# Performance work log

Hardware: AMD Instinct MI355X
Metric: run time of the kernel (lower is better)

Reference implementation:

```python
import jax, jax.numpy as jnp
import numpy as np

N = 50000
E = 800000
F_IN = 128
H = 8        # heads
C = 32       # hidden_channels per head
HC = H * C   # 256
NEG_SLOPE = 0.2


def setup_inputs() -> dict:
    key = jax.random.key(0)
    ks = jax.random.split(key, 16)
    s = 0.1
    return {
        'x': jax.random.normal(ks[0], (N, F_IN), jnp.float32),
        'edge_index': jax.random.randint(ks[1], (2, E), 0, N, jnp.int64),
        'edge_weights': jax.random.uniform(ks[2], (E,), jnp.float32),
        'W1': jax.random.normal(ks[3], (F_IN, HC), jnp.float32) * s,
        'att_src1': jax.random.normal(ks[4], (H, C), jnp.float32) * s,
        'att_dst1': jax.random.normal(ks[5], (H, C), jnp.float32) * s,
        'b1': jnp.zeros((HC,), jnp.float32),
        'W2': jax.random.normal(ks[6], (HC, HC), jnp.float32) * s,
        'att_src2': jax.random.normal(ks[7], (H, C), jnp.float32) * s,
        'att_dst2': jax.random.normal(ks[8], (H, C), jnp.float32) * s,
        'b2': jnp.zeros((HC,), jnp.float32),
        'We': jax.random.normal(ks[9], (HC, 1), jnp.float32) * s,
        'be': jnp.zeros((1,), jnp.float32),
        'Wn': jax.random.normal(ks[10], (HC, 1), jnp.float32) * s,
        'bn': jnp.zeros((1,), jnp.float32),
    }


def gat_conv(x, src, dst, W, att_src, att_dst, bias):
    """PyG GATConv (concat=True, eval mode, self-loops already in src/dst)."""
    n = x.shape[0]
    h = (x @ W).reshape(n, H, C)                      # [N,H,C]
    a_s = jnp.sum(h * att_src, axis=-1)               # [N,H]
    a_d = jnp.sum(h * att_dst, axis=-1)               # [N,H]
    e = jax.nn.leaky_relu(a_s[src] + a_d[dst], NEG_SLOPE)  # [E',H]
    m = jax.ops.segment_max(e, dst, num_segments=n)   # segment softmax over dst
    ex = jnp.exp(e - m[dst])
    denom = jax.ops.segment_sum(ex, dst, num_segments=n)
    alpha = ex / (denom[dst] + 1e-16)                 # [E',H]
    out = jax.ops.segment_sum(alpha[..., None] * h[src], dst, num_segments=n)
    return out.reshape(n, HC) + bias


def reference(x, edge_index, edge_weights, W1, att_src1, att_dst1, b1,
              W2, att_src2, att_dst2, b2, We, be, Wn, bn):
    src0, dst0 = edge_index[0], edge_index[1]
    loops = jnp.arange(N, dtype=src0.dtype)
    src = jnp.concatenate([src0, loops])
    dst = jnp.concatenate([dst0, loops])
    # edge_weights is passed to GATConv as edge_attr but unused (edge_dim=None)
    h = jax.nn.relu(gat_conv(x, src, dst, W1, att_src1, att_dst1, b1))
    h = jax.nn.relu(gat_conv(h, src, dst, W2, att_src2, att_dst2, b2))
    edge_pred = (h[src0] * h[dst0]) @ We + be          # [E,1]
    node_pred = h @ Wn + bn                            # [N,1]
    return (edge_pred, node_pred)
```

## Files before the change

### kernel.cpp

```cpp
#include <hip/hip_runtime.h>
#include <hip/hip_bf16.h>

#define NN 50000
#define NE 800000
#define FIN 128
#define HC 256
#define NEG_SLOPE 0.2f

#define GEMM_BLOCKS 1564
#define NSCAT 3328
#define NB_HIST 782
#define NB_X 6250
#define NB_W1 128
#define NB_W2 256

typedef short bf16x8 __attribute__((ext_vector_type(8)));
typedef float f32x4 __attribute__((ext_vector_type(4)));

__device__ __forceinline__ unsigned short f2bf(float f) {
  unsigned u = __float_as_uint(f);
  u += 0x7fff + ((u >> 16) & 1);
  return (unsigned short)(u >> 16);
}
__device__ __forceinline__ float bf2f(unsigned short s) {
  return __uint_as_float((unsigned)s << 16);
}
__device__ __forceinline__ float bflo(unsigned u) { return __uint_as_float(u << 16); }
__device__ __forceinline__ float bfhi(unsigned u) { return __uint_as_float(u & 0xffff0000u); }

__global__ __launch_bounds__(256) void prep_hist(
    const float* __restrict__ X, unsigned short* __restrict__ Xh,
    const float* __restrict__ W1, unsigned short* __restrict__ W1th,
    unsigned short* __restrict__ W1tl, const float* __restrict__ W2,
    unsigned short* __restrict__ W2th, unsigned short* __restrict__ W2tl,
    const int* __restrict__ ei, int* __restrict__ counts) {
  int b = blockIdx.x, t = threadIdx.x;
  if (b < NB_HIST) {
#pragma unroll
    for (int u = 0; u < 4; ++u) {
      int e = b * 1024 + u * 256 + t;
      if (e < NE) atomicAdd(&counts[ei[NE + e]], 1);
    }
  } else if (b < NB_HIST + NB_X) {
    int i = (b - NB_HIST) * 256 + t;
    float4 v = ((const float4*)X)[i];
    ushort4 h;
    h.x = f2bf(v.x); h.y = f2bf(v.y); h.z = f2bf(v.z); h.w = f2bf(v.w);
    ((ushort4*)Xh)[i] = h;
  } else if (b < NB_HIST + NB_X + NB_W1) {
    int j = (b - NB_HIST - NB_X) * 256 + t;
    int n = j >> 7, k = j & 127;
    float v = W1[k * HC + n];
    unsigned short h = f2bf(v);
    W1th[j] = h;
    W1tl[j] = f2bf(v - bf2f(h));
  } else {
    int j = (b - NB_HIST - NB_X - NB_W1) * 256 + t;
    int n = j >> 8, k = j & 255;
    float v = W2[k * HC + n];
    unsigned short h = f2bf(v);
    W2th[j] = h;
    W2tl[j] = f2bf(v - bf2f(h));
  }
}

__global__ __launch_bounds__(256) void gemm_coef(
    const unsigned short* __restrict__ A, const unsigned short* __restrict__ Bth,
    const unsigned short* __restrict__ Btl, const float* __restrict__ att_s,
    const float* __restrict__ att_d, unsigned short* __restrict__ Cb,
    float* __restrict__ a_s, float* __restrict__ a_d, int M, int K,
    const int* __restrict__ ei, const int* __restrict__ rowptr,
    int* __restrict__ tmpc, int2* __restrict__ ce, int scat) {
  __shared__ unsigned short sA[64 * 40];
  __shared__ unsigned short sBh[128 * 40];
  __shared__ unsigned short sBl[128 * 40];
  __shared__ float sCS[64][4];
  __shared__ float sCD[64][4];

  int bid = blockIdx.x, t = threadIdx.x;
  if (bid < scat) {
    int x = bid & 7;
    int c = bid >> 3;
#pragma unroll
    for (int u = 0; u < 8; ++u) {
      int e = c * 2048 + u * 256 + t;
      if (e < NE + NN) {
        int d = (e < NE) ? ei[NE + e] : e - NE;
        if ((unsigned)d / 6250u == (unsigned)x) {
          int s  = (e < NE) ? ei[e] : d;
          int id = (e < NE) ? e : -1;
          int pos = rowptr[d] + atomicAdd(&tmpc[d], 1);
          ce[pos] = make_int2(s, id);
        }
      }
    }
    return;
  }

  int gb = bid - scat;
  int w = t >> 6, lane = t & 63;
  int quad = lane >> 4, lrow = lane & 15;
  int m0 = (gb >> 1) * 64, n0 = (gb & 1) * 128;
  int rm = (w & 1) * 32, cn = (w >> 1) * 64;

  f32x4 acc[2][4] = {};

  for (int k0 = 0; k0 < K; k0 += 32) {
    {
      int row = t >> 2, q = t & 3;
      int gm = m0 + row;
      if (gm >= M) gm = M - 1;
      *(uint4*)(sA + row * 40 + q * 8) = *(const uint4*)(A + (size_t)gm * K + k0 + q * 8);
    }
#pragma unroll
    for (int i = 0; i < 2; ++i) {
      int idx = t + i * 256;
      int row = idx >> 2, q = idx & 3;
      size_t gbx = (size_t)(n0 + row) * K + k0 + q * 8;
      *(uint4*)(sBh + row * 40 + q * 8) = *(const uint4*)(Bth + gbx);
      *(uint4*)(sBl + row * 40 + q * 8) = *(const uint4*)(Btl + gbx);
    }
    __syncthreads();

    bf16x8 fa[2];
#pragma unroll
    for (int mi = 0; mi < 2; ++mi)
      fa[mi] = *(const bf16x8*)(sA + (rm + mi * 16 + lrow) * 40 + quad * 8);
#pragma unroll
    for (int ni = 0; ni < 4; ++ni) {
      bf16x8 fbh = *(const bf16x8*)(sBh + (cn + ni * 16 + lrow) * 40 + quad * 8);
      bf16x8 fbl = *(const bf16x8*)(sBl + (cn + ni * 16 + lrow) * 40 + quad * 8);
#pragma unroll
      for (int mi = 0; mi < 2; ++mi) {
        acc[mi][ni] = __builtin_amdgcn_mfma_f32_16x16x32_bf16(fa[mi], fbh, acc[mi][ni], 0, 0, 0);
        acc[mi][ni] = __builtin_amdgcn_mfma_f32_16x16x32_bf16(fa[mi], fbl, acc[mi][ni], 0, 0, 0);
      }
    }
    __syncthreads();
  }

  float vs[4], vd[4];
#pragma unroll
  for (int ni = 0; ni < 4; ++ni) {
    int gn = n0 + cn + ni * 16 + lrow;
    vs[ni] = att_s[gn];
    vd[ni] = att_d[gn];
  }
  int h4e = cn >> 5;

#pragma unroll
  for (int mi = 0; mi < 2; ++mi) {
#pragma unroll
    for (int r = 0; r < 4; ++r) {
      int lr = rm + mi * 16 + quad * 4 + r;
      int gm = m0 + lr;
      if (gm < M) {
#pragma unroll
        for (int ni = 0; ni < 4; ++ni) {
          int gn = n0 + cn + ni * 16 + lrow;
          Cb[(size_t)gm * HC + gn] = f2bf(acc[mi][ni][r]);
        }
      }
      float pse = acc[mi][0][r] * vs[0] + acc[mi][1][r] * vs[1];
      float pso = acc[mi][2][r] * vs[2] + acc[mi][3][r] * vs[3];
      float pde = acc[mi][0][r] * vd[0] + acc[mi][1][r] * vd[1];
      float pdo = acc[mi][2][r] * vd[2] + acc[mi][3][r] * vd[3];
#pragma unroll
      for (int off = 1; off <= 8; off <<= 1) {
        pse += __shfl_xor(pse, off);
        pso += __shfl_xor(pso, off);
        pde += __shfl_xor(pde, off);
        pdo += __shfl_xor(pdo, off);
      }
      if (lrow == 0) {
        sCS[lr][h4e] = pse;
        sCS[lr][h4e + 1] = pso;
        sCD[lr][h4e] = pde;
        sCD[lr][h4e + 1] = pdo;
      }
    }
  }
  __syncthreads();
  if (t < 64) {
    int gm = m0 + t;
    if (gm < M) {
      int o = (n0 >> 5);
      *(float4*)(a_s + (size_t)gm * 8 + o) = *(const float4*)&sCS[t][0];
      *(float4*)(a_d + (size_t)gm * 8 + o) = *(const float4*)&sCD[t][0];
    }
  }
}

__global__ void scan1(const int* __restrict__ counts, int* __restrict__ scanbuf,
                      int* __restrict__ bsum) {
  __shared__ int sd[256];
  int t = threadIdx.x;
  int i = blockIdx.x * 256 + t;
  int v = (i < NN) ? counts[i] + 1 : 0;
  sd[t] = v;
  __syncthreads();
#pragma unroll
  for (int off = 1; off < 256; off <<= 1) {
    int x = (t >= off) ? sd[t - off] : 0;
    __syncthreads();
    sd[t] += x;
    __syncthreads();
  }
  if (i < NN) scanbuf[i] = sd[t];
  if (t == 255) bsum[blockIdx.x] = sd[255];
}

__global__ void scan2(const int* __restrict__ bsum, int* __restrict__ boff, int nb) {
  __shared__ int sd[256];
  int t = threadIdx.x;
  int v = (t < nb) ? bsum[t] : 0;
  sd[t] = v;
  __syncthreads();
#pragma unroll
  for (int off = 1; off < 256; off <<= 1) {
    int x = (t >= off) ? sd[t - off] : 0;
    __syncthreads();
    sd[t] += x;
    __syncthreads();
  }
  if (t < nb) boff[t] = sd[t] - v;
}

__global__ void scan3(const int* __restrict__ scanbuf, const int* __restrict__ boff,
                      int* __restrict__ rowptr) {
  int i = blockIdx.x * 256 + threadIdx.x;
  if (i < NN) rowptr[i + 1] = scanbuf[i] + boff[blockIdx.x];
  if (i == 0) rowptr[0] = 0;
}

__global__ __launch_bounds__(256) void agg_kernel(
    const unsigned short* __restrict__ htb, const float* __restrict__ a_s,
    const float* __restrict__ a_d, const int* __restrict__ rowptr,
    const int2* __restrict__ ce, const float* __restrict__ bias,
    unsigned short* __restrict__ outb,
    const float* __restrict__ Wn, const float* __restrict__ bn,
    float* __restrict__ outn) {
  int d = blockIdx.x * 4 + (threadIdx.x >> 6);
  if (d >= NN) return;
  int l = threadIdx.x & 63;
  int hh = l >> 3;
  float adh = a_d[d * 8 + hh];
  int r0 = rowptr[d], r1 = rowptr[d + 1];
  float denom = 0.f;
  float4 acc = {0.f, 0.f, 0.f, 0.f};
  for (int r = r0; r < r1; r += 4) {
    int s[4];
    float as_[4];
    uint2 q[4];
    bool ok[4];
#pragma unroll
    for (int j = 0; j < 4; ++j) {
      int rj = r + j;
      ok[j] = rj < r1;
      rj = ok[j] ? rj : r1 - 1;
      s[j] = ce[rj].x;
    }
#pragma unroll
    for (int j = 0; j < 4; ++j) {
      as_[j] = a_s[s[j] * 8 + hh];
      q[j] = ((const uint2*)(htb + (size_t)s[j] * HC))[l];
    }
#pragma unroll
    for (int j = 0; j < 4; ++j) {
      float e = as_[j] + adh;
      e = e > 0.f ? e : NEG_SLOPE * e;
      float w = ok[j] ? __expf(e) : 0.f;
      denom += w;
      acc.x += w * bflo(q[j].x);
      acc.y += w * bfhi(q[j].x);
      acc.z += w * bflo(q[j].y);
      acc.w += w * bfhi(q[j].y);
    }
  }
  float dv = 1.f / denom;
  float4 bi = *(const float4*)(bias + l * 4);
  float4 o;
  o.x = fmaxf(fmaf(acc.x, dv, bi.x), 0.f);
  o.y = fmaxf(fmaf(acc.y, dv, bi.y), 0.f);
  o.z = fmaxf(fmaf(acc.z, dv, bi.z), 0.f);
  o.w = fmaxf(fmaf(acc.w, dv, bi.w), 0.f);
  uint2 pb;
  pb.x = (unsigned)f2bf(o.x) | ((unsigned)f2bf(o.y) << 16);
  pb.y = (unsigned)f2bf(o.z) | ((unsigned)f2bf(o.w) << 16);
  ((uint2*)(outb + (size_t)d * HC))[l] = pb;
  if (outn) {
    float4 wv = *(const float4*)(Wn + l * 4);
    float p = o.x * wv.x + o.y * wv.y + o.z * wv.z + o.w * wv.w;
#pragma unroll
    for (int off = 1; off <= 32; off <<= 1) p += __shfl_xor(p, off);
    if (l == 0) outn[d] = p + bn[0];
  }
}

__global__ __launch_bounds__(256) void edge_pred_kernel(
    const unsigned short* __restrict__ h2b, const int* __restrict__ rowptr,
    const int2* __restrict__ ce, const float* __restrict__ We,
    const float* __restrict__ be, float* __restrict__ out) {
  int d = blockIdx.x * 4 + (threadIdx.x >> 6);
  if (d >= NN) return;
  int lane = threadIdx.x & 63;
  int g = lane >> 4, l = lane & 15;
  float b = be[0];

  const uint4* rowd = (const uint4*)(h2b + (size_t)d * HC + l * 16);
  uint4 qd0 = rowd[0], qd1 = rowd[1];
  float wd[16];
  {
    const float4* wep = (const float4*)(We + l * 16);
    float4 w0 = wep[0], w1 = wep[1], w2 = wep[2], w3 = wep[3];
    wd[0] = bflo(qd0.x) * w0.x;  wd[1] = bfhi(qd0.x) * w0.y;
    wd[2] = bflo(qd0.y) * w0.z;  wd[3] = bfhi(qd0.y) * w0.w;
    wd[4] = bflo(qd0.z) * w1.x;  wd[5] = bfhi(qd0.z) * w1.y;
    wd[6] = bflo(qd0.w) * w1.z;  wd[7] = bfhi(qd0.w) * w1.w;
    wd[8] = bflo(qd1.x) * w2.x;  wd[9] = bfhi(qd1.x) * w2.y;
    wd[10] = bflo(qd1.y) * w2.z; wd[11] = bfhi(qd1.y) * w2.w;
    wd[12] = bflo(qd1.z) * w3.x; wd[13] = bfhi(qd1.z) * w3.y;
    wd[14] = bflo(qd1.w) * w3.z; wd[15] = bfhi(qd1.w) * w3.w;
  }

  int r0 = rowptr[d], r1 = rowptr[d + 1];
  for (int r = r0; r < r1; r += 8) {
    int rr0 = r + g, rr1 = r + 4 + g;
    int s0 = 0, id0 = -1, s1 = 0, id1 = -1;
    if (rr0 < r1) { int2 p = ce[rr0]; s0 = p.x; id0 = p.y; }
    if (rr1 < r1) { int2 p = ce[rr1]; s1 = p.x; id1 = p.y; }
    const uint4* ra = (const uint4*)(h2b + (size_t)s0 * HC + l * 16);
    const uint4* rb = (const uint4*)(h2b + (size_t)s1 * HC + l * 16);
    uint4 a0 = ra[0], a1 = ra[1];
    uint4 c0 = rb[0], c1 = rb[1];
    float p0 = bflo(a0.x) * wd[0] + bfhi(a0.x) * wd[1] + bflo(a0.y) * wd[2] +
               bfhi(a0.y) * wd[3] + bflo(a0.z) * wd[4] + bfhi(a0.z) * wd[5] +
               bflo(a0.w) * wd[6] + bfhi(a0.w) * wd[7] + bflo(a1.x) * wd[8] +
               bfhi(a1.x) * wd[9] + bflo(a1.y) * wd[10] + bfhi(a1.y) * wd[11] +
               bflo(a1.z) * wd[12] + bfhi(a1.z) * wd[13] + bflo(a1.w) * wd[14] +
               bfhi(a1.w) * wd[15];
    float p1 = bflo(c0.x) * wd[0] + bfhi(c0.x) * wd[1] + bflo(c0.y) * wd[2] +
               bfhi(c0.y) * wd[3] + bflo(c0.z) * wd[4] + bfhi(c0.z) * wd[5] +
               bflo(c0.w) * wd[6] + bfhi(c0.w) * wd[7] + bflo(c1.x) * wd[8] +
               bfhi(c1.x) * wd[9] + bflo(c1.y) * wd[10] + bfhi(c1.y) * wd[11] +
               bflo(c1.z) * wd[12] + bfhi(c1.z) * wd[13] + bflo(c1.w) * wd[14] +
               bfhi(c1.w) * wd[15];
#pragma unroll
    for (int off = 1; off <= 8; off <<= 1) {
      p0 += __shfl_xor(p0, off);
      p1 += __shfl_xor(p1, off);
    }
    if (l == 0) {
      if (id0 >= 0) out[id0] = p0 + b;
      if (id1 >= 0) out[id1] = p1 + b;
    }
  }
}

extern "C" void kernel_launch(void* const* d_in, const int* in_sizes, int n_in,
                              void* d_out, int out_size, void* d_ws, size_t ws_size,
                              hipStream_t stream) {
  const float* x  = (const float*)d_in[0];
  const int* ei   = (const int*)d_in[1];
  const float* W1 = (const float*)d_in[3];
  const float* as1 = (const float*)d_in[4];
  const float* ad1 = (const float*)d_in[5];
  const float* b1 = (const float*)d_in[6];
  const float* W2 = (const float*)d_in[7];
  const float* as2 = (const float*)d_in[8];
  const float* ad2 = (const float*)d_in[9];
  const float* b2 = (const float*)d_in[10];
  const float* We = (const float*)d_in[11];
  const float* be = (const float*)d_in[12];
  const float* Wn = (const float*)d_in[13];
  const float* bn = (const float*)d_in[14];
  float* out = (float*)d_out;

  char* wsp = (char*)d_ws;
  auto alloc = [&](size_t bytes) {
    char* p = wsp;
    wsp += (bytes + 255) & ~(size_t)255;
    return p;
  };
  unsigned short* hbA = (unsigned short*)alloc((size_t)NN * HC * 2);
  unsigned short* h1b = (unsigned short*)alloc((size_t)NN * HC * 2);
  unsigned short* hbB = (unsigned short*)alloc((size_t)NN * HC * 2);
  float* a_s = (float*)alloc((size_t)NN * 8 * 4);
  float* a_d = (float*)alloc((size_t)NN * 8 * 4);
  int* rowptr = (int*)alloc((size_t)(NN + 1) * 4);
  int2* ce = (int2*)alloc((size_t)(NE + NN + 8) * 8);
  int* counts = (int*)alloc((size_t)NN * 4);
  int* tmp = (int*)alloc((size_t)NN * 4);
  int* scanbuf = (int*)alloc((size_t)NN * 4);
  int* bsum = (int*)alloc(256 * 4);
  int* boff = (int*)alloc(256 * 4);
  unsigned short* W1th = (unsigned short*)alloc((size_t)FIN * HC * 2);
  unsigned short* W1tl = (unsigned short*)alloc((size_t)FIN * HC * 2);
  unsigned short* W2th = (unsigned short*)alloc((size_t)HC * HC * 2);
  unsigned short* W2tl = (unsigned short*)alloc((size_t)HC * HC * 2);

  unsigned short* xh = h1b;

  const int NB = (NN + 255) / 256;

  hipMemsetAsync(counts, 0, (size_t)NN * 4, stream);
  hipMemsetAsync(tmp, 0, (size_t)NN * 4, stream);

  prep_hist<<<NB_HIST + NB_X + NB_W1 + NB_W2, 256, 0, stream>>>(
      x, xh, W1, W1th, W1tl, W2, W2th, W2tl, ei, counts);
  scan1<<<NB, 256, 0, stream>>>(counts, scanbuf, bsum);
  scan2<<<1, 256, 0, stream>>>(bsum, boff, NB);
  scan3<<<NB, 256, 0, stream>>>(scanbuf, boff, rowptr);

  gemm_coef<<<NSCAT + GEMM_BLOCKS, 256, 0, stream>>>(
      xh, W1th, W1tl, as1, ad1, hbA, a_s, a_d, NN, FIN, ei, rowptr, tmp, ce, NSCAT);
  agg_kernel<<<NN / 4, 256, 0, stream>>>(hbA, a_s, a_d, rowptr, ce, b1, h1b,
                                         (const float*)nullptr, (const float*)nullptr,
                                         (float*)nullptr);

  gemm_coef<<<GEMM_BLOCKS, 256, 0, stream>>>(
      h1b, W2th, W2tl, as2, ad2, hbA, a_s, a_d, NN, HC,
      (const int*)nullptr, rowptr, tmp, ce, 0);
  agg_kernel<<<NN / 4, 256, 0, stream>>>(hbA, a_s, a_d, rowptr, ce, b2, hbB,
                                         Wn, bn, out + NE);

  edge_pred_kernel<<<NN / 4, 256, 0, stream>>>(hbB, rowptr, ce, We, be, out);
}
```

Before: 439.0 us.

## Pad CSR rows to multiples of four with sentinel edges and persistent agg kernels

Rounds each destination's edge count up to a multiple of four and fills the padding with -1 sentinel sources. Those sources point at a zero feature row and a very negative attention score, so the aggregation inner loop can drop its bounds checks and prefetch the next four indices. Folds log2(e) into the attention vectors so the kernel can use exp2f. Turns the aggregation and edge-prediction kernels into persistent grids that grab four nodes at a time through an atomic work counter. This adds padding memory, an extra memset of the edge list, and atomic contention in exchange for less branching and better load balance.

```diff
diff --git a/kernel.cpp b/kernel.cpp
--- a/kernel.cpp
+++ b/kernel.cpp
@@ -6,6 +6,7 @@
 #define FIN 128
 #define HC 256
 #define NEG_SLOPE 0.2f
+#define LOG2E 1.4426950408889634f
 
 #define GEMM_BLOCKS 1564
 #define NSCAT 3328
@@ -13,6 +14,7 @@
 #define NB_X 6250
 #define NB_W1 128
 #define NB_W2 256
+#define CE_CAP (NE + 4 * NN + 16)
 
 typedef short bf16x8 __attribute__((ext_vector_type(8)));
 typedef float f32x4 __attribute__((ext_vector_type(4)));
@@ -33,7 +35,8 @@
     const float* __restrict__ W1, unsigned short* __restrict__ W1th,
     unsigned short* __restrict__ W1tl, const float* __restrict__ W2,
     unsigned short* __restrict__ W2th, unsigned short* __restrict__ W2tl,
-    const int* __restrict__ ei, int* __restrict__ counts) {
+    const int* __restrict__ ei, int* __restrict__ counts,
+    unsigned* __restrict__ gA, unsigned* __restrict__ gB, float* __restrict__ asg) {
   int b = blockIdx.x, t = threadIdx.x;
   if (b < NB_HIST) {
 #pragma unroll
@@ -54,13 +57,16 @@
     unsigned short h = f2bf(v);
     W1th[j] = h;
     W1tl[j] = f2bf(v - bf2f(h));
-  } else {
+  } else if (b < NB_HIST + NB_X + NB_W1 + NB_W2) {
     int j = (b - NB_HIST - NB_X - NB_W1) * 256 + t;
     int n = j >> 8, k = j & 255;
     float v = W2[k * HC + n];
     unsigned short h = f2bf(v);
     W2th[j] = h;
     W2tl[j] = f2bf(v - bf2f(h));
+  } else {
+    if (t < 128) { gA[t] = 0; gB[t] = 0; }
+    if (t < 8) asg[t] = -1e30f;
   }
 }
 
@@ -143,8 +149,8 @@
 #pragma unroll
   for (int ni = 0; ni < 4; ++ni) {
     int gn = n0 + cn + ni * 16 + lrow;
-    vs[ni] = att_s[gn];
-    vd[ni] = att_d[gn];
+    vs[ni] = att_s[gn] * LOG2E;
+    vd[ni] = att_d[gn] * LOG2E;
   }
   int h4e = cn >> 5;
 
@@ -196,7 +202,7 @@
   __shared__ int sd[256];
   int t = threadIdx.x;
   int i = blockIdx.x * 256 + t;
-  int v = (i < NN) ? counts[i] + 1 : 0;
+  int v = (i < NN) ? ((counts[i] + 1 + 3) & ~3) : 0;
   sd[t] = v;
   __syncthreads();
 #pragma unroll
@@ -233,126 +239,139 @@
   if (i == 0) rowptr[0] = 0;
 }
 
-__global__ __launch_bounds__(256) void agg_kernel(
+__global__ __launch_bounds__(256, 8) void agg_kernel(
     const unsigned short* __restrict__ htb, const float* __restrict__ a_s,
     const float* __restrict__ a_d, const int* __restrict__ rowptr,
     const int2* __restrict__ ce, const float* __restrict__ bias,
     unsigned short* __restrict__ outb,
     const float* __restrict__ Wn, const float* __restrict__ bn,
-    float* __restrict__ outn) {
-  int d = blockIdx.x * 4 + (threadIdx.x >> 6);
-  if (d >= NN) return;
+    float* __restrict__ outn, int* __restrict__ wctr) {
   int l = threadIdx.x & 63;
   int hh = l >> 3;
-  float adh = a_d[d * 8 + hh];
-  int r0 = rowptr[d], r1 = rowptr[d + 1];
-  float denom = 0.f;
-  float4 acc = {0.f, 0.f, 0.f, 0.f};
-  for (int r = r0; r < r1; r += 4) {
-    int s[4];
-    float as_[4];
-    uint2 q[4];
-    bool ok[4];
-#pragma unroll
-    for (int j = 0; j < 4; ++j) {
-      int rj = r + j;
-      ok[j] = rj < r1;
-      rj = ok[j] ? rj : r1 - 1;
-      s[j] = ce[rj].x;
-    }
-#pragma unroll
-    for (int j = 0; j < 4; ++j) {
-      as_[j] = a_s[s[j] * 8 + hh];
-      q[j] = ((const uint2*)(htb + (size_t)s[j] * HC))[l];
-    }
-#pragma unroll
-    for (int j = 0; j < 4; ++j) {
-      float e = as_[j] + adh;
-      e = e > 0.f ? e : NEG_SLOPE * e;
-      float w = ok[j] ? __expf(e) : 0.f;
-      denom += w;
-      acc.x += w * bflo(q[j].x);
-      acc.y += w * bfhi(q[j].x);
-      acc.z += w * bflo(q[j].y);
-      acc.w += w * bfhi(q[j].y);
-    }
-  }
-  float dv = 1.f / denom;
   float4 bi = *(const float4*)(bias + l * 4);
-  float4 o;
-  o.x = fmaxf(fmaf(acc.x, dv, bi.x), 0.f);
-  o.y = fmaxf(fmaf(acc.y, dv, bi.y), 0.f);
-  o.z = fmaxf(fmaf(acc.z, dv, bi.z), 0.f);
-  o.w = fmaxf(fmaf(acc.w, dv, bi.w), 0.f);
-  uint2 pb;
-  pb.x = (unsigned)f2bf(o.x) | ((unsigned)f2bf(o.y) << 16);
-  pb.y = (unsigned)f2bf(o.z) | ((unsigned)f2bf(o.w) << 16);
-  ((uint2*)(outb + (size_t)d * HC))[l] = pb;
-  if (outn) {
-    float4 wv = *(const float4*)(Wn + l * 4);
-    float p = o.x * wv.x + o.y * wv.y + o.z * wv.z + o.w * wv.w;
-#pragma unroll
-    for (int off = 1; off <= 32; off <<= 1) p += __shfl_xor(p, off);
-    if (l == 0) outn[d] = p + bn[0];
+  float4 wv = make_float4(0.f, 0.f, 0.f, 0.f);
+  if (outn) wv = *(const float4*)(Wn + l * 4);
+  const uint2* ht2 = (const uint2*)htb;
+  uint2* ob2 = (uint2*)outb;
+
+  for (;;) {
+    int d0 = 0;
+    if (l == 0) d0 = atomicAdd(wctr, 4);
+    d0 = __shfl(d0, 0);
+    if (d0 >= NN) return;
+    int dend = d0 + 4 < NN ? d0 + 4 : NN;
+    for (int d = d0; d < dend; ++d) {
+      float adh = a_d[d * 8 + hh];
+      int r0 = rowptr[d], r1 = rowptr[d + 1];
+      float denom = 0.f;
+      float4 acc = {0.f, 0.f, 0.f, 0.f};
+      int s0 = ce[r0].x, s1 = ce[r0 + 1].x, s2 = ce[r0 + 2].x, s3 = ce[r0 + 3].x;
+      for (int r = r0; r < r1; r += 4) {
+        int t0 = s0, t1 = s1, t2 = s2, t3 = s3;
+        int rn = r + 4;
+        s0 = ce[rn].x; s1 = ce[rn + 1].x; s2 = ce[rn + 2].x; s3 = ce[rn + 3].x;
+        float as0 = a_s[t0 * 8 + hh], as1 = a_s[t1 * 8 + hh];
+        float as2 = a_s[t2 * 8 + hh], as3 = a_s[t3 * 8 + hh];
+        uint2 q0 = ht2[t0 * 64 + l], q1 = ht2[t1 * 64 + l];
+        uint2 q2 = ht2[t2 * 64 + l], q3 = ht2[t3 * 64 + l];
+        float e0 = as0 + adh; e0 = fmaxf(e0, NEG_SLOPE * e0); float w0 = exp2f(e0);
+        float e1 = as1 + adh; e1 = fmaxf(e1, NEG_SLOPE * e1); float w1 = exp2f(e1);
+        float e2 = as2 + adh; e2 = fmaxf(e2, NEG_SLOPE * e2); float w2 = exp2f(e2);
+        float e3 = as3 + adh; e3 = fmaxf(e3, NEG_SLOPE * e3); float w3 = exp2f(e3);
+        denom += (w0 + w1) + (w2 + w3);
+        acc.x += w0 * bflo(q0.x); acc.y += w0 * bfhi(q0.x);
+        acc.z += w0 * bflo(q0.y); acc.w += w0 * bfhi(q0.y);
+        acc.x += w1 * bflo(q1.x); acc.y += w1 * bfhi(q1.x);
+        acc.z += w1 * bflo(q1.y); acc.w += w1 * bfhi(q1.y);
+        acc.x += w2 * bflo(q2.x); acc.y += w2 * bfhi(q2.x);
+        acc.z += w2 * bflo(q2.y); acc.w += w2 * bfhi(q2.y);
+        acc.x += w3 * bflo(q3.x); acc.y += w3 * bfhi(q3.x);
+        acc.z += w3 * bflo(q3.y); acc.w += w3 * bfhi(q3.y);
+      }
+      float dv = 1.f / denom;
+      float4 o;
+      o.x = fmaxf(fmaf(acc.x, dv, bi.x), 0.f);
+      o.y = fmaxf(fmaf(acc.y, dv, bi.y), 0.f);
+      o.z = fmaxf(fmaf(acc.z, dv, bi.z), 0.f);
+      o.w = fmaxf(fmaf(acc.w, dv, bi.w), 0.f);
+      uint2 pb;
+      pb.x = (unsigned)f2bf(o.x) | ((unsigned)f2bf(o.y) << 16);
+      pb.y = (unsigned)f2bf(o.z) | ((unsigned)f2bf(o.w) << 16);
+      ob2[d * 64 + l] = pb;
+      if (outn) {
+        float p = o.x * wv.x + o.y * wv.y + o.z * wv.z + o.w * wv.w;
+#pragma unroll
+        for (int off = 1; off <= 32; off <<= 1) p += __shfl_xor(p, off);
+        if (l == 0) outn[d] = p + bn[0];
+      }
+    }
   }
 }
 
 __global__ __launch_bounds__(256) void edge_pred_kernel(
     const unsigned short* __restrict__ h2b, const int* __restrict__ rowptr,
     const int2* __restrict__ ce, const float* __restrict__ We,
-    const float* __restrict__ be, float* __restrict__ out) {
-  int d = blockIdx.x * 4 + (threadIdx.x >> 6);
-  if (d >= NN) return;
+    const float* __restrict__ be, float* __restrict__ out, int* __restrict__ wctr) {
   int lane = threadIdx.x & 63;
   int g = lane >> 4, l = lane & 15;
   float b = be[0];
-
-  const uint4* rowd = (const uint4*)(h2b + (size_t)d * HC + l * 16);
-  uint4 qd0 = rowd[0], qd1 = rowd[1];
-  float wd[16];
+  const uint4* h24 = (const uint4*)h2b;
+  float4 w0, w1, w2, w3;
   {
     const float4* wep = (const float4*)(We + l * 16);
-    float4 w0 = wep[0], w1 = wep[1], w2 = wep[2], w3 = wep[3];
-    wd[0] = bflo(qd0.x) * w0.x;  wd[1] = bfhi(qd0.x) * w0.y;
-    wd[2] = bflo(qd0.y) * w0.z;  wd[3] = bfhi(qd0.y) * w0.w;
-    wd[4] = bflo(qd0.z) * w1.x;  wd[5] = bfhi(qd0.z) * w1.y;
-    wd[6] = bflo(qd0.w) * w1.z;  wd[7] = bfhi(qd0.w) * w1.w;
-    wd[8] = bflo(qd1.x) * w2.x;  wd[9] = bfhi(qd1.x) * w2.y;
-    wd[10] = bflo(qd1.y) * w2.z; wd[11] = bfhi(qd1.y) * w2.w;
-    wd[12] = bflo(qd1.z) * w3.x; wd[13] = bfhi(qd1.z) * w3.y;
-    wd[14] = bflo(qd1.w) * w3.z; wd[15] = bfhi(qd1.w) * w3.w;
-  }
-
-  int r0 = rowptr[d], r1 = rowptr[d + 1];
-  for (int r = r0; r < r1; r += 8) {
-    int rr0 = r + g, rr1 = r + 4 + g;
-    int s0 = 0, id0 = -1, s1 = 0, id1 = -1;
-    if (rr0 < r1) { int2 p = ce[rr0]; s0 = p.x; id0 = p.y; }
-    if (rr1 < r1) { int2 p = ce[rr1]; s1 = p.x; id1 = p.y; }
-    const uint4* ra = (const uint4*)(h2b + (size_t)s0 * HC + l * 16);
-    const uint4* rb = (const uint4*)(h2b + (size_t)s1 * HC + l * 16);
-    uint4 a0 = ra[0], a1 = ra[1];
-    uint4 c0 = rb[0], c1 = rb[1];
-    float p0 = bflo(a0.x) * wd[0] + bfhi(a0.x) * wd[1] + bflo(a0.y) * wd[2] +
-               bfhi(a0.y) * wd[3] + bflo(a0.z) * wd[4] + bfhi(a0.z) * wd[5] +
-               bflo(a0.w) * wd[6] + bfhi(a0.w) * wd[7] + bflo(a1.x) * wd[8] +
-               bfhi(a1.x) * wd[9] + bflo(a1.y) * wd[10] + bfhi(a1.y) * wd[11] +
-               bflo(a1.z) * wd[12] + bfhi(a1.z) * wd[13] + bflo(a1.w) * wd[14] +
-               bfhi(a1.w) * wd[15];
-    float p1 = bflo(c0.x) * wd[0] + bfhi(c0.x) * wd[1] + bflo(c0.y) * wd[2] +
-               bfhi(c0.y) * wd[3] + bflo(c0.z) * wd[4] + bfhi(c0.z) * wd[5] +
-               bflo(c0.w) * wd[6] + bfhi(c0.w) * wd[7] + bflo(c1.x) * wd[8] +
-               bfhi(c1.x) * wd[9] + bflo(c1.y) * wd[10] + bfhi(c1.y) * wd[11] +
-               bflo(c1.z) * wd[12] + bfhi(c1.z) * wd[13] + bflo(c1.w) * wd[14] +
-               bfhi(c1.w) * wd[15];
-#pragma unroll
-    for (int off = 1; off <= 8; off <<= 1) {
-      p0 += __shfl_xor(p0, off);
-      p1 += __shfl_xor(p1, off);
-    }
-    if (l == 0) {
-      if (id0 >= 0) out[id0] = p0 + b;
-      if (id1 >= 0) out[id1] = p1 + b;
+    w0 = wep[0]; w1 = wep[1]; w2 = wep[2]; w3 = wep[3];
+  }
+
+  for (;;) {
+    int d0 = 0;
+    if (lane == 0) d0 = atomicAdd(wctr, 4);
+    d0 = __shfl(d0, 0);
+    if (d0 >= NN) return;
+    int dend = d0 + 4 < NN ? d0 + 4 : NN;
+    for (int d = d0; d < dend; ++d) {
+      uint4 qd0 = h24[d * 32 + l * 2], qd1 = h24[d * 32 + l * 2 + 1];
+      float wd[16];
+      wd[0] = bflo(qd0.x) * w0.x;  wd[1] = bfhi(qd0.x) * w0.y;
+      wd[2] = bflo(qd0.y) * w0.z;  wd[3] = bfhi(qd0.y) * w0.w;
+      wd[4] = bflo(qd0.z) * w1.x;  wd[5] = bfhi(qd0.z) * w1.y;
+      wd[6] = bflo(qd0.w) * w1.z;  wd[7] = bfhi(qd0.w) * w1.w;
+      wd[8] = bflo(qd1.x) * w2.x;  wd[9] = bfhi(qd1.x) * w2.y;
+      wd[10] = bflo(qd1.y) * w2.z; wd[11] = bfhi(qd1.y) * w2.w;
+      wd[12] = bflo(qd1.z) * w3.x; wd[13] = bfhi(qd1.z) * w3.y;
+      wd[14] = bflo(qd1.w) * w3.z; wd[15] = bfhi(qd1.w) * w3.w;
+
+      int r0 = rowptr[d], r1 = rowptr[d + 1];
+      for (int r = r0; r < r1; r += 8) {
+        int rr0 = r + g, rr1 = r + 4 + g;
+        int s0 = 0, id0 = -1, s1 = 0, id1 = -1;
+        if (rr0 < r1) { int2 p = ce[rr0]; s0 = p.x; id0 = p.y; }
+        if (rr1 < r1) { int2 p = ce[rr1]; s1 = p.x; id1 = p.y; }
+        if (s0 < 0) s0 = 0;
+        if (s1 < 0) s1 = 0;
+        uint4 a0 = h24[s0 * 32 + l * 2], a1 = h24[s0 * 32 + l * 2 + 1];
+        uint4 c0 = h24[s1 * 32 + l * 2], c1 = h24[s1 * 32 + l * 2 + 1];
+        float p0 = bflo(a0.x) * wd[0] + bfhi(a0.x) * wd[1] + bflo(a0.y) * wd[2] +
+                   bfhi(a0.y) * wd[3] + bflo(a0.z) * wd[4] + bfhi(a0.z) * wd[5] +
+                   bflo(a0.w) * wd[6] + bfhi(a0.w) * wd[7] + bflo(a1.x) * wd[8] +
+                   bfhi(a1.x) * wd[9] + bflo(a1.y) * wd[10] + bfhi(a1.y) * wd[11] +
+                   bflo(a1.z) * wd[12] + bfhi(a1.z) * wd[13] + bflo(a1.w) * wd[14] +
+                   bfhi(a1.w) * wd[15];
+        float p1 = bflo(c0.x) * wd[0] + bfhi(c0.x) * wd[1] + bflo(c0.y) * wd[2] +
+                   bfhi(c0.y) * wd[3] + bflo(c0.z) * wd[4] + bfhi(c0.z) * wd[5] +
+                   bflo(c0.w) * wd[6] + bfhi(c0.w) * wd[7] + bflo(c1.x) * wd[8] +
+                   bfhi(c1.x) * wd[9] + bflo(c1.y) * wd[10] + bfhi(c1.y) * wd[11] +
+                   bflo(c1.z) * wd[12] + bfhi(c1.z) * wd[13] + bflo(c1.w) * wd[14] +
+                   bfhi(c1.w) * wd[15];
+#pragma unroll
+        for (int off = 1; off <= 8; off <<= 1) {
+          p0 += __shfl_xor(p0, off);
+          p1 += __shfl_xor(p1, off);
+        }
+        if (l == 0) {
+          if (id0 >= 0) out[id0] = p0 + b;
+          if (id1 >= 0) out[id1] = p1 + b;
+        }
+      }
     }
   }
 }
@@ -382,15 +401,19 @@
     wsp += (bytes + 255) & ~(size_t)255;
     return p;
   };
-  unsigned short* hbA = (unsigned short*)alloc((size_t)NN * HC * 2);
+  unsigned short* hbAr = (unsigned short*)alloc((size_t)(NN + 1) * HC * 2);
+  unsigned short* hbA = hbAr + HC;
   unsigned short* h1b = (unsigned short*)alloc((size_t)NN * HC * 2);
-  unsigned short* hbB = (unsigned short*)alloc((size_t)NN * HC * 2);
-  float* a_s = (float*)alloc((size_t)NN * 8 * 4);
+  unsigned short* hbBr = (unsigned short*)alloc((size_t)(NN + 1) * HC * 2);
+  unsigned short* hbB = hbBr + HC;
+  float* a_sr = (float*)alloc((size_t)(8 + NN * 8) * 4);
+  float* a_s = a_sr + 8;
   float* a_d = (float*)alloc((size_t)NN * 8 * 4);
   int* rowptr = (int*)alloc((size_t)(NN + 1) * 4);
-  int2* ce = (int2*)alloc((size_t)(NE + NN + 8) * 8);
+  int2* ce = (int2*)alloc((size_t)CE_CAP * 8);
   int* counts = (int*)alloc((size_t)NN * 4);
   int* tmp = (int*)alloc((size_t)NN * 4);
+  int* ctrs = (int*)alloc(256);
   int* scanbuf = (int*)alloc((size_t)NN * 4);
   int* bsum = (int*)alloc(256 * 4);
   int* boff = (int*)alloc(256 * 4);
@@ -403,26 +426,27 @@
 
   const int NB = (NN + 255) / 256;
 
-  hipMemsetAsync(counts, 0, (size_t)NN * 4, stream);
-  hipMemsetAsync(tmp, 0, (size_t)NN * 4, stream);
-
-  prep_hist<<<NB_HIST + NB_X + NB_W1 + NB_W2, 256, 0, stream>>>(
-      x, xh, W1, W1th, W1tl, W2, W2th, W2tl, ei, counts);
+  hipMemsetAsync(counts, 0, (size_t)((char*)(ctrs + 64) - (char*)counts), stream);
+  hipMemsetAsync(ce, 0xFF, (size_t)CE_CAP * 8, stream);
+
+  prep_hist<<<NB_HIST + NB_X + NB_W1 + NB_W2 + 1, 256, 0, stream>>>(
+      x, xh, W1, W1th, W1tl, W2, W2th, W2tl, ei, counts,
+      (unsigned*)hbAr, (unsigned*)hbBr, a_sr);
   scan1<<<NB, 256, 0, stream>>>(counts, scanbuf, bsum);
   scan2<<<1, 256, 0, stream>>>(bsum, boff, NB);
   scan3<<<NB, 256, 0, stream>>>(scanbuf, boff, rowptr);
 
   gemm_coef<<<NSCAT + GEMM_BLOCKS, 256, 0, stream>>>(
       xh, W1th, W1tl, as1, ad1, hbA, a_s, a_d, NN, FIN, ei, rowptr, tmp, ce, NSCAT);
-  agg_kernel<<<NN / 4, 256, 0, stream>>>(hbA, a_s, a_d, rowptr, ce, b1, h1b,
-                                         (const float*)nullptr, (const float*)nullptr,
-                                         (float*)nullptr);
+  agg_kernel<<<2048, 256, 0, stream>>>(hbA, a_s, a_d, rowptr, ce, b1, h1b,
+                                       (const float*)nullptr, (const float*)nullptr,
+                                       (float*)nullptr, ctrs + 0);
 
   gemm_coef<<<GEMM_BLOCKS, 256, 0, stream>>>(
       h1b, W2th, W2tl, as2, ad2, hbA, a_s, a_d, NN, HC,
       (const int*)nullptr, rowptr, tmp, ce, 0);
-  agg_kernel<<<NN / 4, 256, 0, stream>>>(hbA, a_s, a_d, rowptr, ce, b2, hbB,
-                                         Wn, bn, out + NE);
-
-  edge_pred_kernel<<<NN / 4, 256, 0, stream>>>(hbB, rowptr, ce, We, be, out);
-}
+  agg_kernel<<<2048, 256, 0, stream>>>(hbA, a_s, a_d, rowptr, ce, b2, hbB,
+                                       Wn, bn, out + NE, ctrs + 1);
+
+  edge_pred_kernel<<<2048, 256, 0, stream>>>(hbB, rowptr, ce, We, be, out, ctrs + 2);
+}
```

New measurement: 1.039 ms. 2.37x slower.

## Pad CSR rows to multiples of four with sentinel edges to drop tail masking

Applied to the files above, without the earlier changes.

Each destination row in the CSR is padded to a multiple of four entries. The padding entries are memset to -1, so they index a zeroed guard row placed before the feature buffers and an a_s guard entry of -1e30, which makes their softmax weight zero. This removes the per-edge bounds checks and select logic in the aggregation loop. Attention vectors are also prescaled by log2(e) so exp2f can replace __expf, and the two memsets of counts and tmp are merged into one. In exchange it adds a large memset of the padded edge array, more edge slots to process, and reliance on the -1 sentinel indexing.

```diff
diff --git a/kernel.cpp b/kernel.cpp
--- a/kernel.cpp
+++ b/kernel.cpp
@@ -6,6 +6,7 @@
 #define FIN 128
 #define HC 256
 #define NEG_SLOPE 0.2f
+#define LOG2E 1.4426950408889634f
 
 #define GEMM_BLOCKS 1564
 #define NSCAT 3328
@@ -13,6 +14,7 @@
 #define NB_X 6250
 #define NB_W1 128
 #define NB_W2 256
+#define CE_CAP (NE + 4 * NN + 16)
 
 typedef short bf16x8 __attribute__((ext_vector_type(8)));
 typedef float f32x4 __attribute__((ext_vector_type(4)));
@@ -33,7 +35,8 @@
     const float* __restrict__ W1, unsigned short* __restrict__ W1th,
     unsigned short* __restrict__ W1tl, const float* __restrict__ W2,
     unsigned short* __restrict__ W2th, unsigned short* __restrict__ W2tl,
-    const int* __restrict__ ei, int* __restrict__ counts) {
+    const int* __restrict__ ei, int* __restrict__ counts,
+    unsigned* __restrict__ gA, unsigned* __restrict__ gB, float* __restrict__ asg) {
   int b = blockIdx.x, t = threadIdx.x;
   if (b < NB_HIST) {
 #pragma unroll
@@ -54,13 +57,16 @@
     unsigned short h = f2bf(v);
     W1th[j] = h;
     W1tl[j] = f2bf(v - bf2f(h));
-  } else {
+  } else if (b < NB_HIST + NB_X + NB_W1 + NB_W2) {
     int j = (b - NB_HIST - NB_X - NB_W1) * 256 + t;
     int n = j >> 8, k = j & 255;
     float v = W2[k * HC + n];
     unsigned short h = f2bf(v);
     W2th[j] = h;
     W2tl[j] = f2bf(v - bf2f(h));
+  } else {
+    if (t < 128) { gA[t] = 0; gB[t] = 0; }
+    if (t < 8) asg[t] = -1e30f;
   }
 }
 
@@ -143,8 +149,8 @@
 #pragma unroll
   for (int ni = 0; ni < 4; ++ni) {
     int gn = n0 + cn + ni * 16 + lrow;
-    vs[ni] = att_s[gn];
-    vd[ni] = att_d[gn];
+    vs[ni] = att_s[gn] * LOG2E;
+    vd[ni] = att_d[gn] * LOG2E;
   }
   int h4e = cn >> 5;
 
@@ -196,7 +202,7 @@
   __shared__ int sd[256];
   int t = threadIdx.x;
   int i = blockIdx.x * 256 + t;
-  int v = (i < NN) ? counts[i] + 1 : 0;
+  int v = (i < NN) ? ((counts[i] + 1 + 3) & ~3) : 0;
   sd[t] = v;
   __syncthreads();
 #pragma unroll
@@ -244,32 +250,27 @@
   if (d >= NN) return;
   int l = threadIdx.x & 63;
   int hh = l >> 3;
+  const uint2* ht2 = (const uint2*)htb;
   float adh = a_d[d * 8 + hh];
   int r0 = rowptr[d], r1 = rowptr[d + 1];
   float denom = 0.f;
   float4 acc = {0.f, 0.f, 0.f, 0.f};
   for (int r = r0; r < r1; r += 4) {
     int s[4];
+#pragma unroll
+    for (int j = 0; j < 4; ++j) s[j] = ce[r + j].x;
     float as_[4];
     uint2 q[4];
-    bool ok[4];
-#pragma unroll
-    for (int j = 0; j < 4; ++j) {
-      int rj = r + j;
-      ok[j] = rj < r1;
-      rj = ok[j] ? rj : r1 - 1;
-      s[j] = ce[rj].x;
-    }
 #pragma unroll
     for (int j = 0; j < 4; ++j) {
       as_[j] = a_s[s[j] * 8 + hh];
-      q[j] = ((const uint2*)(htb + (size_t)s[j] * HC))[l];
+      q[j] = ht2[s[j] * 64 + l];
     }
 #pragma unroll
     for (int j = 0; j < 4; ++j) {
       float e = as_[j] + adh;
-      e = e > 0.f ? e : NEG_SLOPE * e;
-      float w = ok[j] ? __expf(e) : 0.f;
+      e = fmaxf(e, NEG_SLOPE * e);
+      float w = exp2f(e);
       denom += w;
       acc.x += w * bflo(q[j].x);
       acc.y += w * bfhi(q[j].x);
@@ -287,7 +288,7 @@
   uint2 pb;
   pb.x = (unsigned)f2bf(o.x) | ((unsigned)f2bf(o.y) << 16);
   pb.y = (unsigned)f2bf(o.z) | ((unsigned)f2bf(o.w) << 16);
-  ((uint2*)(outb + (size_t)d * HC))[l] = pb;
+  ((uint2*)outb)[d * 64 + l] = pb;
   if (outn) {
     float4 wv = *(const float4*)(Wn + l * 4);
     float p = o.x * wv.x + o.y * wv.y + o.z * wv.z + o.w * wv.w;
@@ -306,9 +307,9 @@
   int lane = threadIdx.x & 63;
   int g = lane >> 4, l = lane & 15;
   float b = be[0];
-
-  const uint4* rowd = (const uint4*)(h2b + (size_t)d * HC + l * 16);
-  uint4 qd0 = rowd[0], qd1 = rowd[1];
+  const uint4* h24 = (const uint4*)h2b;
+
+  uint4 qd0 = h24[d * 32 + l * 2], qd1 = h24[d * 32 + l * 2 + 1];
   float wd[16];
   {
     const float4* wep = (const float4*)(We + l * 16);
@@ -329,10 +330,8 @@
     int s0 = 0, id0 = -1, s1 = 0, id1 = -1;
     if (rr0 < r1) { int2 p = ce[rr0]; s0 = p.x; id0 = p.y; }
     if (rr1 < r1) { int2 p = ce[rr1]; s1 = p.x; id1 = p.y; }
-    const uint4* ra = (const uint4*)(h2b + (size_t)s0 * HC + l * 16);
-    const uint4* rb = (const uint4*)(h2b + (size_t)s1 * HC + l * 16);
-    uint4 a0 = ra[0], a1 = ra[1];
-    uint4 c0 = rb[0], c1 = rb[1];
+    uint4 a0 = h24[s0 * 32 + l * 2], a1 = h24[s0 * 32 + l * 2 + 1];
+    uint4 c0 = h24[s1 * 32 + l * 2], c1 = h24[s1 * 32 + l * 2 + 1];
     float p0 = bflo(a0.x) * wd[0] + bfhi(a0.x) * wd[1] + bflo(a0.y) * wd[2] +
                bfhi(a0.y) * wd[3] + bflo(a0.z) * wd[4] + bfhi(a0.z) * wd[5] +
                bflo(a0.w) * wd[6] + bfhi(a0.w) * wd[7] + bflo(a1.x) * wd[8] +
@@ -382,13 +381,16 @@
     wsp += (bytes + 255) & ~(size_t)255;
     return p;
   };
-  unsigned short* hbA = (unsigned short*)alloc((size_t)NN * HC * 2);
+  unsigned short* hbAr = (unsigned short*)alloc((size_t)(NN + 1) * HC * 2);
+  unsigned short* hbA = hbAr + HC;
   unsigned short* h1b = (unsigned short*)alloc((size_t)NN * HC * 2);
-  unsigned short* hbB = (unsigned short*)alloc((size_t)NN * HC * 2);
-  float* a_s = (float*)alloc((size_t)NN * 8 * 4);
+  unsigned short* hbBr = (unsigned short*)alloc((size_t)(NN + 1) * HC * 2);
+  unsigned short* hbB = hbBr + HC;
+  float* a_sr = (float*)alloc((size_t)(8 + NN * 8) * 4);
+  float* a_s = a_sr + 8;
   float* a_d = (float*)alloc((size_t)NN * 8 * 4);
   int* rowptr = (int*)alloc((size_t)(NN + 1) * 4);
-  int2* ce = (int2*)alloc((size_t)(NE + NN + 8) * 8);
+  int2* ce = (int2*)alloc((size_t)CE_CAP * 8);
   int* counts = (int*)alloc((size_t)NN * 4);
   int* tmp = (int*)alloc((size_t)NN * 4);
   int* scanbuf = (int*)alloc((size_t)NN * 4);
@@ -403,11 +405,13 @@
 
   const int NB = (NN + 255) / 256;
 
-  hipMemsetAsync(counts, 0, (size_t)NN * 4, stream);
-  hipMemsetAsync(tmp, 0, (size_t)NN * 4, stream);
-
-  prep_hist<<<NB_HIST + NB_X + NB_W1 + NB_W2, 256, 0, stream>>>(
-      x, xh, W1, W1th, W1tl, W2, W2th, W2tl, ei, counts);
+  hipMemsetAsync(counts, 0,
+                 (size_t)((char*)tmp - (char*)counts) + (size_t)NN * 4, stream);
+  hipMemsetAsync(ce, 0xFF, (size_t)CE_CAP * 8, stream);
+
+  prep_hist<<<NB_HIST + NB_X + NB_W1 + NB_W2 + 1, 256, 0, stream>>>(
+      x, xh, W1, W1th, W1tl, W2, W2th, W2tl, ei, counts,
+      (unsigned*)hbAr, (unsigned*)hbBr, a_sr);
   scan1<<<NB, 256, 0, stream>>>(counts, scanbuf, bsum);
   scan2<<<1, 256, 0, stream>>>(bsum, boff, NB);
   scan3<<<NB, 256, 0, stream>>>(scanbuf, boff, rowptr);
```

Measured after the change: 436.0 us. Within noise of the previous version (-0.7%).
